# Performance work log

Measured on AMD Instinct MI355X. Metric: run time of the kernel, lower is better.

## Reference

```python
import jax, jax.numpy as jnp
import numpy as np

N = 50000
E = 800000
D_IN = 384
D_H = 128
D_MLP = 128
K = 16


def layer_norm(x, g, b, eps=1e-5):
    m = x.mean(-1, keepdims=True)
    v = ((x - m) ** 2).mean(-1, keepdims=True)
    return (x - m) / jnp.sqrt(v + eps) * g + b


def setup_inputs() -> dict:
    key = jax.random.key(0)
    ks = jax.random.split(key, 16)
    s = lambda d: 1.0 / np.sqrt(d)
    return {
        "x": jax.random.normal(ks[0], (N, D_IN), jnp.float32),
        "edge_index": jax.random.randint(ks[1], (2, E), 0, N, jnp.int64),
        # GCNConv 1
        "W1": jax.random.normal(ks[2], (D_IN, D_H), jnp.float32) * s(D_IN),
        "b1": jnp.zeros((D_H,), jnp.float32),
        "g1": jnp.ones((D_H,), jnp.float32),
        "be1": jnp.zeros((D_H,), jnp.float32),
        # GCNConv 2
        "W2": jax.random.normal(ks[3], (D_H, D_H), jnp.float32) * s(D_H),
        "b2": jnp.zeros((D_H,), jnp.float32),
        "g2": jnp.ones((D_H,), jnp.float32),
        "be2": jnp.zeros((D_H,), jnp.float32),
        # residual projection (input_dim != conv_hidden)
        "rW": jax.random.normal(ks[4], (D_IN, D_H), jnp.float32) * s(D_IN),
        "rb": jnp.zeros((D_H,), jnp.float32),
        "rg": jnp.ones((D_H,), jnp.float32),
        "rbe": jnp.zeros((D_H,), jnp.float32),
        # MLP head
        "mW1": jax.random.normal(ks[5], (D_H, D_MLP), jnp.float32) * s(D_H),
        "mb1": jnp.zeros((D_MLP,), jnp.float32),
        "mg": jnp.ones((D_MLP,), jnp.float32),
        "mbe": jnp.zeros((D_MLP,), jnp.float32),
        "mW2": jax.random.normal(ks[6], (D_MLP, K), jnp.float32) * s(D_MLP),
        "mb2": jnp.zeros((K,), jnp.float32),
    }


def reference(x, edge_index, W1, b1, g1, be1, W2, b2, g2, be2,
              rW, rb, rg, rbe, mW1, mb1, mg, mbe, mW2, mb2):
    n = x.shape[0]
    loops = jnp.arange(n, dtype=edge_index.dtype)
    src = jnp.concatenate([edge_index[0], loops])  # [E+N]
    dst = jnp.concatenate([edge_index[1], loops])
    # symmetric GCN normalization with self-loops
    deg = jax.ops.segment_sum(jnp.ones_like(src, x.dtype), dst, num_segments=n)
    dinv = jnp.where(deg > 0, jax.lax.rsqrt(deg), 0.0)
    norm = dinv[src] * dinv[dst]  # [E+N]

    def gcn_conv(h, W, b):
        hw = h @ W  # [N, D_H]
        msg = hw[src] * norm[:, None]  # gather + scale, [E+N, D_H]
        return jax.ops.segment_sum(msg, dst, num_segments=n) + b

    # layer 1 with projected residual
    h = jax.nn.elu(layer_norm(gcn_conv(x, W1, b1), g1, be1))
    h = h + layer_norm(x @ rW + rb, rg, rbe)
    # layer 2 with identity residual
    h = jax.nn.elu(layer_norm(gcn_conv(h, W2, b2), g2, be2)) + h
    # MLP head (dropout inactive in eval) + softmax over clusters
    z = jax.nn.elu(layer_norm(h @ mW1 + mb1, mg, mbe))
    H = z @ mW2 + mb2
    return jax.nn.softmax(H, axis=1)
```

## Files before the change

### kernel.cpp

```cpp
#include <hip/hip_runtime.h>

#define DH 128

typedef __attribute__((ext_vector_type(8))) short short8;
typedef __attribute__((ext_vector_type(4))) float f32x4;

__device__ __forceinline__ float wave_sum(float v) {
    #pragma unroll
    for (int o = 32; o > 0; o >>= 1) v += __shfl_xor(v, o, 64);
    return v;
}

__device__ __forceinline__ void ln_pair(float v0, float v1, float& o0, float& o1) {
    float m = wave_sum(v0 + v1) * (1.f / 128.f);
    float d0 = v0 - m, d1 = v1 - m;
    float var = wave_sum(d0 * d0 + d1 * d1) * (1.f / 128.f);
    float inv = rsqrtf(var + 1e-5f);
    o0 = d0 * inv; o1 = d1 * inv;
}

__device__ __forceinline__ float elu(float x) { return x > 0.f ? x : expm1f(x); }

__device__ __forceinline__ unsigned short f2bf(float f) {
    unsigned u = __float_as_uint(f);
    u += 0x7fffu + ((u >> 16) & 1u);
    return (unsigned short)(u >> 16);
}
__device__ __forceinline__ float bfl(unsigned u) { return __uint_as_float(u << 16); }
__device__ __forceinline__ float bfh(unsigned u) { return __uint_as_float(u & 0xffff0000u); }
__device__ __forceinline__ unsigned pack_bf2(float a, float b) {
    return (unsigned)f2bf(a) | ((unsigned)f2bf(b) << 16);
}

__global__ void zero_int_k(int* __restrict__ p, int n) {
    int i = blockIdx.x * 256 + threadIdx.x;
    if (i < n) p[i] = 0;
}

__global__ void deg_count_k(const int* __restrict__ dst, int* __restrict__ deg, int E) {
    int e = blockIdx.x * 256 + threadIdx.x;
    if (e < E) atomicAdd(&deg[dst[e]], 1);
}

__global__ void dinv_k(const int* __restrict__ deg, float* __restrict__ dinv, int n) {
    int i = blockIdx.x * 256 + threadIdx.x;
    if (i < n) dinv[i] = rsqrtf((float)(deg[i] + 1));
}

__global__ __launch_bounds__(1024) void scan_k(const int* __restrict__ deg,
                                               int* __restrict__ rowptr,
                                               int* __restrict__ cursor, int n)
{
    __shared__ int wsum[16];
    __shared__ int carry;
    const int tid = threadIdx.x, lane = tid & 63, wid = tid >> 6;
    if (tid == 0) carry = 0;
    __syncthreads();
    for (int base = 0; base < n; base += 1024) {
        int i = base + tid;
        int v = (i < n) ? deg[i] : 0;
        int s = v;
        #pragma unroll
        for (int o = 1; o < 64; o <<= 1) {
            int t = __shfl_up(s, o, 64);
            if (lane >= o) s += t;
        }
        if (lane == 63) wsum[wid] = s;
        __syncthreads();
        if (tid < 16) {
            int ws = wsum[tid];
            #pragma unroll
            for (int o = 1; o < 16; o <<= 1) {
                int t = __shfl_up(ws, o, 64);
                if (tid >= o) ws += t;
            }
            wsum[tid] = ws;
        }
        __syncthreads();
        int excl = carry + (wid ? wsum[wid - 1] : 0) + s - v;
        if (i < n) { rowptr[i] = excl; cursor[i] = excl; }
        int tot = wsum[15];
        __syncthreads();
        if (tid == 0) carry += tot;
        __syncthreads();
    }
    if (threadIdx.x == 0) rowptr[n] = carry;
}

__global__ void fill_k(const int* __restrict__ src, const int* __restrict__ dst,
                       const float* __restrict__ dinv, int* __restrict__ cursor,
                       int2* __restrict__ csr, int E)
{
    int e = blockIdx.x * 256 + threadIdx.x;
    if (e < E) {
        int s = src[e], d = dst[e];
        float w = dinv[s] * dinv[d];
        int p = atomicAdd(&cursor[d], 1);
        csr[p] = make_int2(s, __float_as_int(w));
    }
}

__global__ void repack_w_k(const float* __restrict__ W, unsigned short* __restrict__ Wp, int K) {
    int idx = blockIdx.x * 256 + threadIdx.x;
    if (idx >= K * DH) return;
    int kb  = idx / (DH * 32);
    int rem = idx - kb * (DH * 32);
    int nn  = rem >> 5;
    int ki  = rem & 31;
    Wp[idx] = f2bf(W[(kb * 32 + ki) * DH + nn]);
}

template<int K, bool DUAL, bool AF32>
__global__ __launch_bounds__(256) void mfma_gemm(
    const void* __restrict__ Av,
    const unsigned short* __restrict__ Bp1, const float* __restrict__ ba,
    const unsigned short* __restrict__ Bp2, const float* __restrict__ bb,
    unsigned short* __restrict__ outa, unsigned short* __restrict__ outb, int n)
{
    constexpr int LDA = 40;
    __shared__ unsigned short smem[64 * LDA + (DUAL ? 2 : 1) * 128 * LDA];
    unsigned short* As  = smem;
    unsigned short* Bs1 = smem + 64 * LDA;
    unsigned short* Bs2 = smem + 64 * LDA + 128 * LDA;

    const int tid  = threadIdx.x;
    const int wid  = tid >> 6, lane = tid & 63;
    const int wr   = wid >> 1, wc = wid & 1;
    const int m16  = lane & 15, q = lane >> 4;
    const long long rowbase = (long long)blockIdx.x * 64;

    f32x4 acc1[2][4], acc2[2][4];
    const f32x4 zero = {0.f, 0.f, 0.f, 0.f};
    #pragma unroll
    for (int i = 0; i < 2; i++)
        #pragma unroll
        for (int j = 0; j < 4; j++) { acc1[i][j] = zero; if constexpr (DUAL) acc2[i][j] = zero; }

    const int ar = tid >> 2, akq = tid & 3;
    long long gr = rowbase + ar; if (gr >= n) gr = n - 1;

    for (int kb = 0; kb < K / 32; ++kb) {
        if constexpr (AF32) {
            const float* A = (const float*)Av;
            const float* ap = A + gr * K + kb * 32 + akq * 8;
            float4 v0 = *(const float4*)(ap);
            float4 v1 = *(const float4*)(ap + 4);
            short8 o;
            o[0] = (short)f2bf(v0.x); o[1] = (short)f2bf(v0.y);
            o[2] = (short)f2bf(v0.z); o[3] = (short)f2bf(v0.w);
            o[4] = (short)f2bf(v1.x); o[5] = (short)f2bf(v1.y);
            o[6] = (short)f2bf(v1.z); o[7] = (short)f2bf(v1.w);
            *(short8*)(As + ar * LDA + akq * 8) = o;
        } else {
            const unsigned short* A = (const unsigned short*)Av;
            short8 o = *(const short8*)(A + gr * K + kb * 32 + akq * 8);
            *(short8*)(As + ar * LDA + akq * 8) = o;
        }
        #pragma unroll
        for (int h = 0; h < 2; ++h) {
            int cb = tid + h * 256;
            int rb_ = cb >> 2, kqb = cb & 3;
            short8 w1 = *(const short8*)(Bp1 + (long long)kb * 4096 + cb * 8);
            *(short8*)(Bs1 + rb_ * LDA + kqb * 8) = w1;
            if constexpr (DUAL) {
                short8 w2 = *(const short8*)(Bp2 + (long long)kb * 4096 + cb * 8);
                *(short8*)(Bs2 + rb_ * LDA + kqb * 8) = w2;
            }
        }
        __syncthreads();

        short8 af[2], bfr1[4], bfr2[4];
        #pragma unroll
        for (int mi = 0; mi < 2; ++mi)
            af[mi] = *(const short8*)(As + (wr * 32 + mi * 16 + m16) * LDA + q * 8);
        #pragma unroll
        for (int nj = 0; nj < 4; ++nj) {
            bfr1[nj] = *(const short8*)(Bs1 + (wc * 64 + nj * 16 + m16) * LDA + q * 8);
            if constexpr (DUAL)
                bfr2[nj] = *(const short8*)(Bs2 + (wc * 64 + nj * 16 + m16) * LDA + q * 8);
        }
        #pragma unroll
        for (int mi = 0; mi < 2; ++mi)
            #pragma unroll
            for (int nj = 0; nj < 4; ++nj) {
                acc1[mi][nj] = __builtin_amdgcn_mfma_f32_16x16x32_bf16(af[mi], bfr1[nj], acc1[mi][nj], 0, 0, 0);
                if constexpr (DUAL)
                    acc2[mi][nj] = __builtin_amdgcn_mfma_f32_16x16x32_bf16(af[mi], bfr2[nj], acc2[mi][nj], 0, 0, 0);
            }
        __syncthreads();
    }

    #pragma unroll
    for (int nj = 0; nj < 4; ++nj) {
        int col = wc * 64 + nj * 16 + m16;
        float bav = ba ? ba[col] : 0.f;
        float bbv = 0.f;
        if constexpr (DUAL) bbv = bb ? bb[col] : 0.f;
        #pragma unroll
        for (int mi = 0; mi < 2; ++mi) {
            long long row0 = rowbase + wr * 32 + mi * 16 + q * 4;
            #pragma unroll
            for (int r = 0; r < 4; ++r) {
                long long rr = row0 + r;
                if (rr < n) {
                    outa[rr * DH + col] = f2bf(acc1[mi][nj][r] + bav);
                    if constexpr (DUAL) outb[rr * DH + col] = f2bf(acc2[mi][nj][r] + bbv);
                }
            }
        }
    }
}

__device__ __forceinline__ void gather_row(
    const unsigned* __restrict__ hw, const int2* __restrict__ csr,
    int beg, int end, int lane, float& a0, float& a1)
{
    a0 = 0.f; a1 = 0.f;
    float b0 = 0.f, b1v = 0.f, c0 = 0.f, c1 = 0.f, d0 = 0.f, d1 = 0.f;
    int p = beg;
    for (; p + 3 < end; p += 4) {
        int2 e0 = csr[p], e1 = csr[p + 1], e2 = csr[p + 2], e3 = csr[p + 3];
        unsigned u0 = hw[(long long)e0.x * 64 + lane];
        unsigned u1 = hw[(long long)e1.x * 64 + lane];
        unsigned u2 = hw[(long long)e2.x * 64 + lane];
        unsigned u3 = hw[(long long)e3.x * 64 + lane];
        float w0 = __int_as_float(e0.y), w1 = __int_as_float(e1.y);
        float w2 = __int_as_float(e2.y), w3 = __int_as_float(e3.y);
        a0 = fmaf(w0, bfl(u0), a0);   a1 = fmaf(w0, bfh(u0), a1);
        b0 = fmaf(w1, bfl(u1), b0);   b1v = fmaf(w1, bfh(u1), b1v);
        c0 = fmaf(w2, bfl(u2), c0);   c1 = fmaf(w2, bfh(u2), c1);
        d0 = fmaf(w3, bfl(u3), d0);   d1 = fmaf(w3, bfh(u3), d1);
    }
    for (; p < end; ++p) {
        int2 e0 = csr[p];
        unsigned u0 = hw[(long long)e0.x * 64 + lane];
        float w0 = __int_as_float(e0.y);
        a0 = fmaf(w0, bfl(u0), a0);
        a1 = fmaf(w0, bfh(u0), a1);
    }
    a0 += b0 + c0 + d0;
    a1 += b1v + c1 + d1;
}

__global__ __launch_bounds__(256) void gfuse1_k(
    const unsigned* __restrict__ hw, const unsigned* __restrict__ proj,
    const int* __restrict__ rowptr, const int2* __restrict__ csr,
    const float* __restrict__ dinv,
    const float* __restrict__ b1, const float* __restrict__ g1, const float* __restrict__ be1,
    const float* __restrict__ rg, const float* __restrict__ rbe,
    unsigned* __restrict__ hout, int n)
{
    int row = blockIdx.x * 4 + (threadIdx.x >> 6);
    if (row >= n) return;
    int lane = threadIdx.x & 63;
    float a0, a1;
    gather_row(hw, csr, rowptr[row], rowptr[row + 1], lane, a0, a1);
    long long off = (long long)row * 64;
    float di = dinv[row], sl = di * di;
    unsigned us = hw[off + lane];
    float2 bv  = *(const float2*)(b1 + 2 * lane);
    float2 gv  = *(const float2*)(g1 + 2 * lane);
    float2 bev = *(const float2*)(be1 + 2 * lane);
    float2 rgv = *(const float2*)(rg + 2 * lane);
    float2 rbv = *(const float2*)(rbe + 2 * lane);
    float v0 = a0 + sl * bfl(us) + bv.x;
    float v1 = a1 + sl * bfh(us) + bv.y;
    float o0, o1; ln_pair(v0, v1, o0, o1);
    float t0 = elu(o0 * gv.x + bev.x);
    float t1 = elu(o1 * gv.y + bev.y);
    unsigned up = proj[off + lane];
    float q0, q1; ln_pair(bfl(up), bfh(up), q0, q1);
    hout[off + lane] = pack_bf2(t0 + q0 * rgv.x + rbv.x, t1 + q1 * rgv.y + rbv.y);
}

__global__ __launch_bounds__(256) void gfuse2_k(
    const unsigned* __restrict__ hw, const unsigned* __restrict__ hprev,
    const int* __restrict__ rowptr, const int2* __restrict__ csr,
    const float* __restrict__ dinv,
    const float* __restrict__ b2, const float* __restrict__ g2, const float* __restrict__ be2,
    unsigned* __restrict__ h2, int n)
{
    int row = blockIdx.x * 4 + (threadIdx.x >> 6);
    if (row >= n) return;
    int lane = threadIdx.x & 63;
    float a0, a1;
    gather_row(hw, csr, rowptr[row], rowptr[row + 1], lane, a0, a1);
    long long off = (long long)row * 64;
    float di = dinv[row], sl = di * di;
    unsigned us = hw[off + lane];
    float2 bv  = *(const float2*)(b2 + 2 * lane);
    float2 gv  = *(const float2*)(g2 + 2 * lane);
    float2 bev = *(const float2*)(be2 + 2 * lane);
    float v0 = a0 + sl * bfl(us) + bv.x;
    float v1 = a1 + sl * bfh(us) + bv.y;
    float o0, o1; ln_pair(v0, v1, o0, o1);
    float t0 = elu(o0 * gv.x + bev.x);
    float t1 = elu(o1 * gv.y + bev.y);
    unsigned uh = hprev[off + lane];
    h2[off + lane] = pack_bf2(t0 + bfl(uh), t1 + bfh(uh));
}

__global__ __launch_bounds__(256) void ln_elu_k(
    const unsigned* __restrict__ in, const float* __restrict__ g, const float* __restrict__ be,
    unsigned* __restrict__ outp, int n)
{
    int row = blockIdx.x * 4 + (threadIdx.x >> 6);
    if (row >= n) return;
    int lane = threadIdx.x & 63;
    long long off = (long long)row * 64;
    unsigned u = in[off + lane];
    float o0, o1; ln_pair(bfl(u), bfh(u), o0, o1);
    float2 gv  = *(const float2*)(g + 2 * lane);
    float2 bev = *(const float2*)(be + 2 * lane);
    outp[off + lane] = pack_bf2(elu(o0 * gv.x + bev.x), elu(o1 * gv.y + bev.y));
}

__global__ __launch_bounds__(256) void final_k(
    const unsigned* __restrict__ z, const float* __restrict__ mW2, const float* __restrict__ mb2,
    float* __restrict__ out, int n)
{
    int row = blockIdx.x * 4 + (threadIdx.x >> 6);
    if (row >= n) return;
    int lane = threadIdx.x & 63;
    int k = lane & 15, seg = lane >> 4;
    const unsigned* zr = z + (long long)row * 64 + seg * 16;
    float acc = 0.f;
    #pragma unroll
    for (int jj = 0; jj < 16; jj++) {
        unsigned u = zr[jj];
        int c = seg * 32 + 2 * jj;
        acc = fmaf(bfl(u), mW2[c * 16 + k], acc);
        acc = fmaf(bfh(u), mW2[(c + 1) * 16 + k], acc);
    }
    acc += __shfl_xor(acc, 32, 64);
    acc += __shfl_xor(acc, 16, 64);
    float hk = acc + mb2[k];
    float mx = hk;
    #pragma unroll
    for (int o = 8; o > 0; o >>= 1) mx = fmaxf(mx, __shfl_xor(mx, o, 64));
    float e = expf(hk - mx);
    float s = e;
    #pragma unroll
    for (int o = 8; o > 0; o >>= 1) s += __shfl_xor(s, o, 64);
    if (lane < 16) out[(long long)row * 16 + k] = e / s;
}

static inline size_t align16(size_t x) { return (x + 15) & ~(size_t)15; }

extern "C" void kernel_launch(void* const* d_in, const int* in_sizes, int n_in,
                              void* d_out, int out_size, void* d_ws, size_t ws_size,
                              hipStream_t stream)
{
    const float* x   = (const float*)d_in[0];
    const int*   ei  = (const int*)d_in[1];
    const float* W1  = (const float*)d_in[2];
    const float* b1  = (const float*)d_in[3];
    const float* g1  = (const float*)d_in[4];
    const float* be1 = (const float*)d_in[5];
    const float* W2  = (const float*)d_in[6];
    const float* b2  = (const float*)d_in[7];
    const float* g2  = (const float*)d_in[8];
    const float* be2 = (const float*)d_in[9];
    const float* rW  = (const float*)d_in[10];
    const float* rb  = (const float*)d_in[11];
    const float* rg  = (const float*)d_in[12];
    const float* rbe = (const float*)d_in[13];
    const float* mW1 = (const float*)d_in[14];
    const float* mb1 = (const float*)d_in[15];
    const float* mg  = (const float*)d_in[16];
    const float* mbe = (const float*)d_in[17];
    const float* mW2 = (const float*)d_in[18];
    const float* mb2 = (const float*)d_in[19];
    float* out = (float*)d_out;

    const int n = in_sizes[0] / 384;
    const int E = in_sizes[1] / 2;
    const int* src = ei;
    const int* dst = ei + E;

    char* w = (char*)d_ws;
    int* deg     = (int*)w;   w += align16((size_t)n * 4);
    int* rowptr  = (int*)w;   w += align16((size_t)(n + 1) * 4);
    int* cursor  = (int*)w;   w += align16((size_t)n * 4);
    float* dinv  = (float*)w; w += align16((size_t)n * 4);
    int2* csr    = (int2*)w;  w += align16((size_t)E * 8);
    unsigned short* hw1  = (unsigned short*)w; w += align16((size_t)n * DH * 2);
    unsigned short* proj = (unsigned short*)w; w += align16((size_t)n * DH * 2);
    unsigned short* hbuf = (unsigned short*)w; w += align16((size_t)n * DH * 2);
    unsigned short* Wp1 = (unsigned short*)w; w += align16((size_t)384 * DH * 2);
    unsigned short* Wpr = (unsigned short*)w; w += align16((size_t)384 * DH * 2);
    unsigned short* Wp2 = (unsigned short*)w; w += align16((size_t)128 * DH * 2);
    unsigned short* WpM = (unsigned short*)w; w += align16((size_t)128 * DH * 2);
    unsigned short* hw2  = hw1;
    unsigned short* h2   = proj;
    unsigned short* zraw = hbuf;
    unsigned short* zbuf = hw1;

    int gE = (E + 255) / 256;
    int gN = (n + 255) / 256;
    int gG = (n + 63) / 64;
    int gRow4 = (n + 3) / 4;

    zero_int_k<<<gN, 256, 0, stream>>>(deg, n);
    deg_count_k<<<gE, 256, 0, stream>>>(dst, deg, E);
    dinv_k<<<gN, 256, 0, stream>>>(deg, dinv, n);
    scan_k<<<1, 1024, 0, stream>>>(deg, rowptr, cursor, n);
    fill_k<<<gE, 256, 0, stream>>>(src, dst, dinv, cursor, csr, E);

    repack_w_k<<<(384 * DH + 255) / 256, 256, 0, stream>>>(W1, Wp1, 384);
    repack_w_k<<<(384 * DH + 255) / 256, 256, 0, stream>>>(rW, Wpr, 384);
    repack_w_k<<<(128 * DH + 255) / 256, 256, 0, stream>>>(W2, Wp2, 128);
    repack_w_k<<<(128 * DH + 255) / 256, 256, 0, stream>>>(mW1, WpM, 128);

    mfma_gemm<384, true, true><<<gG, 256, 0, stream>>>(x, Wp1, nullptr, Wpr, rb, hw1, proj, n);
    gfuse1_k<<<gRow4, 256, 0, stream>>>((unsigned*)hw1, (unsigned*)proj, rowptr, csr, dinv,
                                        b1, g1, be1, rg, rbe, (unsigned*)hbuf, n);

    mfma_gemm<128, false, false><<<gG, 256, 0, stream>>>(hbuf, Wp2, nullptr, nullptr, nullptr, hw2, nullptr, n);
    gfuse2_k<<<gRow4, 256, 0, stream>>>((unsigned*)hw2, (unsigned*)hbuf, rowptr, csr, dinv,
                                        b2, g2, be2, (unsigned*)h2, n);

    mfma_gemm<128, false, false><<<gG, 256, 0, stream>>>(h2, WpM, mb1, nullptr, nullptr, zraw, nullptr, n);
    ln_elu_k<<<gRow4, 256, 0, stream>>>((unsigned*)zraw, mg, mbe, (unsigned*)zbuf, n);
    final_k<<<gRow4, 256, 0, stream>>>((unsigned*)zbuf, mW2, mb2, out, n);
}
```

Measured before the change: 478.8 us.

## Parallelize CSR scan, register-pipeline GEMM, widen gather unroll, fuse head kernels

Result: faster. 449.4 us (-6.1%).

```diff
diff --git a/kernel.cpp b/kernel.cpp
--- a/kernel.cpp
+++ b/kernel.cpp
@@ -31,6 +31,14 @@
 __device__ __forceinline__ unsigned pack_bf2(float a, float b) {
     return (unsigned)f2bf(a) | ((unsigned)f2bf(b) << 16);
 }
+__device__ __forceinline__ short8 cvt8(float4 v0, float4 v1) {
+    short8 o;
+    o[0] = (short)f2bf(v0.x); o[1] = (short)f2bf(v0.y);
+    o[2] = (short)f2bf(v0.z); o[3] = (short)f2bf(v0.w);
+    o[4] = (short)f2bf(v1.x); o[5] = (short)f2bf(v1.y);
+    o[6] = (short)f2bf(v1.z); o[7] = (short)f2bf(v1.w);
+    return o;
+}
 
 __global__ void zero_int_k(int* __restrict__ p, int n) {
     int i = blockIdx.x * 256 + threadIdx.x;
@@ -47,44 +55,64 @@
     if (i < n) dinv[i] = rsqrtf((float)(deg[i] + 1));
 }
 
-__global__ __launch_bounds__(1024) void scan_k(const int* __restrict__ deg,
-                                               int* __restrict__ rowptr,
-                                               int* __restrict__ cursor, int n)
+__global__ __launch_bounds__(1024) void scan_part_k(const int* __restrict__ deg,
+                                                    int* __restrict__ rowptr,
+                                                    int* __restrict__ bsum, int n)
 {
     __shared__ int wsum[16];
-    __shared__ int carry;
     const int tid = threadIdx.x, lane = tid & 63, wid = tid >> 6;
-    if (tid == 0) carry = 0;
+    int i = blockIdx.x * 1024 + tid;
+    int v = (i < n) ? deg[i] : 0;
+    int s = v;
+    #pragma unroll
+    for (int o = 1; o < 64; o <<= 1) {
+        int t = __shfl_up(s, o, 64);
+        if (lane >= o) s += t;
+    }
+    if (lane == 63) wsum[wid] = s;
     __syncthreads();
-    for (int base = 0; base < n; base += 1024) {
-        int i = base + tid;
-        int v = (i < n) ? deg[i] : 0;
+    if (tid < 16) {
+        int ws = wsum[tid];
+        #pragma unroll
+        for (int o = 1; o < 16; o <<= 1) {
+            int t = __shfl_up(ws, o, 64);
+            if (tid >= o) ws += t;
+        }
+        wsum[tid] = ws;
+    }
+    __syncthreads();
+    int excl = (wid ? wsum[wid - 1] : 0) + s - v;
+    if (i < n) rowptr[i] = excl;
+    if (tid == 0) bsum[blockIdx.x] = wsum[15];
+}
+
+__global__ void scan_top_k(int* __restrict__ bsum, int* __restrict__ rowptr_n, int nb) {
+    int lane = threadIdx.x;
+    int carry = 0;
+    for (int base = 0; base < nb; base += 64) {
+        int i = base + lane;
+        int v = (i < nb) ? bsum[i] : 0;
         int s = v;
         #pragma unroll
         for (int o = 1; o < 64; o <<= 1) {
             int t = __shfl_up(s, o, 64);
             if (lane >= o) s += t;
         }
-        if (lane == 63) wsum[wid] = s;
-        __syncthreads();
-        if (tid < 16) {
-            int ws = wsum[tid];
-            #pragma unroll
-            for (int o = 1; o < 16; o <<= 1) {
-                int t = __shfl_up(ws, o, 64);
-                if (tid >= o) ws += t;
-            }
-            wsum[tid] = ws;
-        }
-        __syncthreads();
-        int excl = carry + (wid ? wsum[wid - 1] : 0) + s - v;
-        if (i < n) { rowptr[i] = excl; cursor[i] = excl; }
-        int tot = wsum[15];
-        __syncthreads();
-        if (tid == 0) carry += tot;
-        __syncthreads();
-    }
-    if (threadIdx.x == 0) rowptr[n] = carry;
+        if (i < nb) bsum[i] = carry + s - v;
+        carry += __shfl(s, 63, 64);
+    }
+    if (lane == 0) *rowptr_n = carry;
+}
+
+__global__ void scan_add_k(const int* __restrict__ bsum, int* __restrict__ rowptr,
+                           int* __restrict__ cursor, int n)
+{
+    int i = blockIdx.x * 256 + threadIdx.x;
+    if (i < n) {
+        int v = rowptr[i] + bsum[i >> 10];
+        rowptr[i] = v;
+        cursor[i] = v;
+    }
 }
 
 __global__ void fill_k(const int* __restrict__ src, const int* __restrict__ dst,
@@ -117,17 +145,18 @@
     const unsigned short* __restrict__ Bp2, const float* __restrict__ bb,
     unsigned short* __restrict__ outa, unsigned short* __restrict__ outb, int n)
 {
-    constexpr int LDA = 40;
-    __shared__ unsigned short smem[64 * LDA + (DUAL ? 2 : 1) * 128 * LDA];
-    unsigned short* As  = smem;
-    unsigned short* Bs1 = smem + 64 * LDA;
-    unsigned short* Bs2 = smem + 64 * LDA + 128 * LDA;
-
-    const int tid  = threadIdx.x;
-    const int wid  = tid >> 6, lane = tid & 63;
-    const int wr   = wid >> 1, wc = wid & 1;
-    const int m16  = lane & 15, q = lane >> 4;
-    const long long rowbase = (long long)blockIdx.x * 64;
+    constexpr int NKB = K / 32;
+    const int tid = threadIdx.x;
+    const int wid = tid >> 6, lane = tid & 63;
+    const int m16 = lane & 15, q = lane >> 4;
+    const long long rb0 = (long long)blockIdx.x * 128 + wid * 32;
+    const int colb = blockIdx.y * 64;
+
+    long long r0 = rb0 + m16;      if (r0 > (long long)n - 1) r0 = n - 1;
+    long long r1 = rb0 + 16 + m16; if (r1 > (long long)n - 1) r1 = n - 1;
+
+    const float* Af = (const float*)Av;
+    const unsigned short* Ah = (const unsigned short*)Av;
 
     f32x4 acc1[2][4], acc2[2][4];
     const f32x4 zero = {0.f, 0.f, 0.f, 0.f};
@@ -136,69 +165,60 @@
         #pragma unroll
         for (int j = 0; j < 4; j++) { acc1[i][j] = zero; if constexpr (DUAL) acc2[i][j] = zero; }
 
-    const int ar = tid >> 2, akq = tid & 3;
-    long long gr = rowbase + ar; if (gr >= n) gr = n - 1;
-
-    for (int kb = 0; kb < K / 32; ++kb) {
+    float4 ra[2][2][2];
+    short8 ha[2][2];
+    short8 pb1[2][4], pb2[2][4];
+
+    auto fetch = [&](int kb, int buf) {
         if constexpr (AF32) {
-            const float* A = (const float*)Av;
-            const float* ap = A + gr * K + kb * 32 + akq * 8;
-            float4 v0 = *(const float4*)(ap);
-            float4 v1 = *(const float4*)(ap + 4);
-            short8 o;
-            o[0] = (short)f2bf(v0.x); o[1] = (short)f2bf(v0.y);
-            o[2] = (short)f2bf(v0.z); o[3] = (short)f2bf(v0.w);
-            o[4] = (short)f2bf(v1.x); o[5] = (short)f2bf(v1.y);
-            o[6] = (short)f2bf(v1.z); o[7] = (short)f2bf(v1.w);
-            *(short8*)(As + ar * LDA + akq * 8) = o;
+            const float* p0 = Af + r0 * K + kb * 32 + q * 8;
+            const float* p1 = Af + r1 * K + kb * 32 + q * 8;
+            ra[buf][0][0] = *(const float4*)p0;  ra[buf][0][1] = *(const float4*)(p0 + 4);
+            ra[buf][1][0] = *(const float4*)p1;  ra[buf][1][1] = *(const float4*)(p1 + 4);
         } else {
-            const unsigned short* A = (const unsigned short*)Av;
-            short8 o = *(const short8*)(A + gr * K + kb * 32 + akq * 8);
-            *(short8*)(As + ar * LDA + akq * 8) = o;
-        }
-        #pragma unroll
-        for (int h = 0; h < 2; ++h) {
-            int cb = tid + h * 256;
-            int rb_ = cb >> 2, kqb = cb & 3;
-            short8 w1 = *(const short8*)(Bp1 + (long long)kb * 4096 + cb * 8);
-            *(short8*)(Bs1 + rb_ * LDA + kqb * 8) = w1;
-            if constexpr (DUAL) {
-                short8 w2 = *(const short8*)(Bp2 + (long long)kb * 4096 + cb * 8);
-                *(short8*)(Bs2 + rb_ * LDA + kqb * 8) = w2;
-            }
-        }
-        __syncthreads();
-
-        short8 af[2], bfr1[4], bfr2[4];
-        #pragma unroll
-        for (int mi = 0; mi < 2; ++mi)
-            af[mi] = *(const short8*)(As + (wr * 32 + mi * 16 + m16) * LDA + q * 8);
+            ha[buf][0] = *(const short8*)(Ah + r0 * K + kb * 32 + q * 8);
+            ha[buf][1] = *(const short8*)(Ah + r1 * K + kb * 32 + q * 8);
+        }
         #pragma unroll
         for (int nj = 0; nj < 4; ++nj) {
-            bfr1[nj] = *(const short8*)(Bs1 + (wc * 64 + nj * 16 + m16) * LDA + q * 8);
-            if constexpr (DUAL)
-                bfr2[nj] = *(const short8*)(Bs2 + (wc * 64 + nj * 16 + m16) * LDA + q * 8);
+            long long boff = ((long long)kb * 128 + colb + nj * 16 + m16) * 32 + q * 8;
+            pb1[buf][nj] = *(const short8*)(Bp1 + boff);
+            if constexpr (DUAL) pb2[buf][nj] = *(const short8*)(Bp2 + boff);
+        }
+    };
+
+    fetch(0, 0);
+    #pragma unroll
+    for (int kb = 0; kb < NKB; ++kb) {
+        const int cur = kb & 1, nxt = cur ^ 1;
+        if (kb + 1 < NKB) fetch(kb + 1, nxt);
+        short8 af[2];
+        if constexpr (AF32) {
+            af[0] = cvt8(ra[cur][0][0], ra[cur][0][1]);
+            af[1] = cvt8(ra[cur][1][0], ra[cur][1][1]);
+        } else {
+            af[0] = ha[cur][0];
+            af[1] = ha[cur][1];
         }
         #pragma unroll
         for (int mi = 0; mi < 2; ++mi)
             #pragma unroll
             for (int nj = 0; nj < 4; ++nj) {
-                acc1[mi][nj] = __builtin_amdgcn_mfma_f32_16x16x32_bf16(af[mi], bfr1[nj], acc1[mi][nj], 0, 0, 0);
+                acc1[mi][nj] = __builtin_amdgcn_mfma_f32_16x16x32_bf16(af[mi], pb1[cur][nj], acc1[mi][nj], 0, 0, 0);
                 if constexpr (DUAL)
-                    acc2[mi][nj] = __builtin_amdgcn_mfma_f32_16x16x32_bf16(af[mi], bfr2[nj], acc2[mi][nj], 0, 0, 0);
+                    acc2[mi][nj] = __builtin_amdgcn_mfma_f32_16x16x32_bf16(af[mi], pb2[cur][nj], acc2[mi][nj], 0, 0, 0);
             }
-        __syncthreads();
     }
 
     #pragma unroll
     for (int nj = 0; nj < 4; ++nj) {
-        int col = wc * 64 + nj * 16 + m16;
+        int col = colb + nj * 16 + m16;
         float bav = ba ? ba[col] : 0.f;
         float bbv = 0.f;
         if constexpr (DUAL) bbv = bb ? bb[col] : 0.f;
         #pragma unroll
         for (int mi = 0; mi < 2; ++mi) {
-            long long row0 = rowbase + wr * 32 + mi * 16 + q * 4;
+            long long row0 = rb0 + mi * 16 + q * 4;
             #pragma unroll
             for (int r = 0; r < 4; ++r) {
                 long long rr = row0 + r;
@@ -213,11 +233,35 @@
 
 __device__ __forceinline__ void gather_row(
     const unsigned* __restrict__ hw, const int2* __restrict__ csr,
-    int beg, int end, int lane, float& a0, float& a1)
-{
-    a0 = 0.f; a1 = 0.f;
-    float b0 = 0.f, b1v = 0.f, c0 = 0.f, c1 = 0.f, d0 = 0.f, d1 = 0.f;
+    int beg, int end, int lane, float& o0, float& o1)
+{
+    float a0 = 0.f, a1 = 0.f, b0 = 0.f, b1 = 0.f;
+    float c0 = 0.f, c1 = 0.f, d0 = 0.f, d1 = 0.f;
     int p = beg;
+    for (; p + 7 < end; p += 8) {
+        int2 e0 = csr[p],     e1 = csr[p + 1], e2 = csr[p + 2], e3 = csr[p + 3];
+        int2 e4 = csr[p + 4], e5 = csr[p + 5], e6 = csr[p + 6], e7 = csr[p + 7];
+        unsigned u0 = hw[(long long)e0.x * 64 + lane];
+        unsigned u1 = hw[(long long)e1.x * 64 + lane];
+        unsigned u2 = hw[(long long)e2.x * 64 + lane];
+        unsigned u3 = hw[(long long)e3.x * 64 + lane];
+        unsigned u4 = hw[(long long)e4.x * 64 + lane];
+        unsigned u5 = hw[(long long)e5.x * 64 + lane];
+        unsigned u6 = hw[(long long)e6.x * 64 + lane];
+        unsigned u7 = hw[(long long)e7.x * 64 + lane];
+        float w0 = __int_as_float(e0.y), w1 = __int_as_float(e1.y);
+        float w2 = __int_as_float(e2.y), w3 = __int_as_float(e3.y);
+        float w4 = __int_as_float(e4.y), w5 = __int_as_float(e5.y);
+        float w6 = __int_as_float(e6.y), w7 = __int_as_float(e7.y);
+        a0 = fmaf(w0, bfl(u0), a0);  a1 = fmaf(w0, bfh(u0), a1);
+        b0 = fmaf(w1, bfl(u1), b0);  b1 = fmaf(w1, bfh(u1), b1);
+        c0 = fmaf(w2, bfl(u2), c0);  c1 = fmaf(w2, bfh(u2), c1);
+        d0 = fmaf(w3, bfl(u3), d0);  d1 = fmaf(w3, bfh(u3), d1);
+        a0 = fmaf(w4, bfl(u4), a0);  a1 = fmaf(w4, bfh(u4), a1);
+        b0 = fmaf(w5, bfl(u5), b0);  b1 = fmaf(w5, bfh(u5), b1);
+        c0 = fmaf(w6, bfl(u6), c0);  c1 = fmaf(w6, bfh(u6), c1);
+        d0 = fmaf(w7, bfl(u7), d0);  d1 = fmaf(w7, bfh(u7), d1);
+    }
     for (; p + 3 < end; p += 4) {
         int2 e0 = csr[p], e1 = csr[p + 1], e2 = csr[p + 2], e3 = csr[p + 3];
         unsigned u0 = hw[(long long)e0.x * 64 + lane];
@@ -226,10 +270,10 @@
         unsigned u3 = hw[(long long)e3.x * 64 + lane];
         float w0 = __int_as_float(e0.y), w1 = __int_as_float(e1.y);
         float w2 = __int_as_float(e2.y), w3 = __int_as_float(e3.y);
-        a0 = fmaf(w0, bfl(u0), a0);   a1 = fmaf(w0, bfh(u0), a1);
-        b0 = fmaf(w1, bfl(u1), b0);   b1v = fmaf(w1, bfh(u1), b1v);
-        c0 = fmaf(w2, bfl(u2), c0);   c1 = fmaf(w2, bfh(u2), c1);
-        d0 = fmaf(w3, bfl(u3), d0);   d1 = fmaf(w3, bfh(u3), d1);
+        a0 = fmaf(w0, bfl(u0), a0);  a1 = fmaf(w0, bfh(u0), a1);
+        b0 = fmaf(w1, bfl(u1), b0);  b1 = fmaf(w1, bfh(u1), b1);
+        c0 = fmaf(w2, bfl(u2), c0);  c1 = fmaf(w2, bfh(u2), c1);
+        d0 = fmaf(w3, bfl(u3), d0);  d1 = fmaf(w3, bfh(u3), d1);
     }
     for (; p < end; ++p) {
         int2 e0 = csr[p];
@@ -238,8 +282,8 @@
         a0 = fmaf(w0, bfl(u0), a0);
         a1 = fmaf(w0, bfh(u0), a1);
     }
-    a0 += b0 + c0 + d0;
-    a1 += b1v + c1 + d1;
+    o0 = (a0 + b0) + (c0 + d0);
+    o1 = (a1 + b1) + (c1 + d1);
 }
 
 __global__ __launch_bounds__(256) void gfuse1_k(
@@ -300,37 +344,30 @@
     h2[off + lane] = pack_bf2(t0 + bfl(uh), t1 + bfh(uh));
 }
 
-__global__ __launch_bounds__(256) void ln_elu_k(
-    const unsigned* __restrict__ in, const float* __restrict__ g, const float* __restrict__ be,
-    unsigned* __restrict__ outp, int n)
+__global__ __launch_bounds__(256) void head_k(
+    const unsigned* __restrict__ zraw, const float* __restrict__ g, const float* __restrict__ be,
+    const float* __restrict__ mW2, const float* __restrict__ mb2,
+    float* __restrict__ out, int n)
 {
     int row = blockIdx.x * 4 + (threadIdx.x >> 6);
     if (row >= n) return;
     int lane = threadIdx.x & 63;
-    long long off = (long long)row * 64;
-    unsigned u = in[off + lane];
+    unsigned u = zraw[(long long)row * 64 + lane];
     float o0, o1; ln_pair(bfl(u), bfh(u), o0, o1);
     float2 gv  = *(const float2*)(g + 2 * lane);
     float2 bev = *(const float2*)(be + 2 * lane);
-    outp[off + lane] = pack_bf2(elu(o0 * gv.x + bev.x), elu(o1 * gv.y + bev.y));
-}
-
-__global__ __launch_bounds__(256) void final_k(
-    const unsigned* __restrict__ z, const float* __restrict__ mW2, const float* __restrict__ mb2,
-    float* __restrict__ out, int n)
-{
-    int row = blockIdx.x * 4 + (threadIdx.x >> 6);
-    if (row >= n) return;
-    int lane = threadIdx.x & 63;
+    float z0 = elu(o0 * gv.x + bev.x);
+    float z1 = elu(o1 * gv.y + bev.y);
     int k = lane & 15, seg = lane >> 4;
-    const unsigned* zr = z + (long long)row * 64 + seg * 16;
     float acc = 0.f;
     #pragma unroll
-    for (int jj = 0; jj < 16; jj++) {
-        unsigned u = zr[jj];
-        int c = seg * 32 + 2 * jj;
-        acc = fmaf(bfl(u), mW2[c * 16 + k], acc);
-        acc = fmaf(bfh(u), mW2[(c + 1) * 16 + k], acc);
+    for (int t = 0; t < 16; ++t) {
+        int srcl = seg * 16 + t;
+        float zz0 = __shfl(z0, srcl, 64);
+        float zz1 = __shfl(z1, srcl, 64);
+        int c = seg * 32 + 2 * t;
+        acc = fmaf(zz0, mW2[c * 16 + k], acc);
+        acc = fmaf(zz1, mW2[(c + 1) * 16 + k], acc);
     }
     acc += __shfl_xor(acc, 32, 64);
     acc += __shfl_xor(acc, 16, 64);
@@ -383,6 +420,7 @@
     int* rowptr  = (int*)w;   w += align16((size_t)(n + 1) * 4);
     int* cursor  = (int*)w;   w += align16((size_t)n * 4);
     float* dinv  = (float*)w; w += align16((size_t)n * 4);
+    int* bsum    = (int*)w;   w += align16((size_t)1024 * 4);
     int2* csr    = (int2*)w;  w += align16((size_t)E * 8);
     unsigned short* hw1  = (unsigned short*)w; w += align16((size_t)n * DH * 2);
     unsigned short* proj = (unsigned short*)w; w += align16((size_t)n * DH * 2);
@@ -394,17 +432,19 @@
     unsigned short* hw2  = hw1;
     unsigned short* h2   = proj;
     unsigned short* zraw = hbuf;
-    unsigned short* zbuf = hw1;
 
     int gE = (E + 255) / 256;
     int gN = (n + 255) / 256;
-    int gG = (n + 63) / 64;
+    int nb = (n + 1023) / 1024;
+    dim3 gG((n + 127) / 128, 2);
     int gRow4 = (n + 3) / 4;
 
     zero_int_k<<<gN, 256, 0, stream>>>(deg, n);
     deg_count_k<<<gE, 256, 0, stream>>>(dst, deg, E);
     dinv_k<<<gN, 256, 0, stream>>>(deg, dinv, n);
-    scan_k<<<1, 1024, 0, stream>>>(deg, rowptr, cursor, n);
+    scan_part_k<<<nb, 1024, 0, stream>>>(deg, rowptr, bsum, n);
+    scan_top_k<<<1, 64, 0, stream>>>(bsum, rowptr + n, nb);
+    scan_add_k<<<gN, 256, 0, stream>>>(bsum, rowptr, cursor, n);
     fill_k<<<gE, 256, 0, stream>>>(src, dst, dinv, cursor, csr, E);
 
     repack_w_k<<<(384 * DH + 255) / 256, 256, 0, stream>>>(W1, Wp1, 384);
@@ -421,6 +461,5 @@
                                         b2, g2, be2, (unsigned*)h2, n);
 
     mfma_gemm<128, false, false><<<gG, 256, 0, stream>>>(h2, WpM, mb1, nullptr, nullptr, zraw, nullptr, n);
-    ln_elu_k<<<gRow4, 256, 0, stream>>>((unsigned*)zraw, mg, mbe, (unsigned*)zbuf, n);
-    final_k<<<gRow4, 256, 0, stream>>>((unsigned*)zbuf, mW2, mb2, out, n);
-}
+    head_k<<<gRow4, 256, 0, stream>>>((unsigned*)zraw, mg, mbe, mW2, mb2, out, n);
+}
```
